# Kernel optimization log

Hardware: AMD Instinct MI355X
Metric: run time of the kernel (lower is better)

The kernel has to match this reference:

```python
import jax, jax.numpy as jnp
import numpy as np
import math

B, S, D, H = 2, 2048, 1024, 16
DK = D // H
SCALE = math.sqrt(DK)
NEG_BIG = -1e9


def setup_inputs() -> dict:
    key = jax.random.key(0)
    ks = jax.random.split(key, 7)
    x = jax.random.normal(ks[0], (B, S, D), dtype=jnp.float32)
    # additive causal mask: 0 on/below diagonal, -inf above
    causal = jnp.triu(jnp.ones((S, S), dtype=bool), k=1)
    mask = jnp.where(causal, -jnp.inf, 0.0).astype(jnp.float32)
    key_padding_mask = jax.random.bernoulli(ks[1], 0.1, (B, S))
    init = 1.0 / math.sqrt(D)
    Wq = jax.random.normal(ks[2], (D, D), dtype=jnp.float32) * init
    Wk = jax.random.normal(ks[3], (D, D), dtype=jnp.float32) * init
    Wv = jax.random.normal(ks[4], (D, D), dtype=jnp.float32) * init
    Wo = jax.random.normal(ks[5], (D, D), dtype=jnp.float32) * init
    bo = jnp.zeros((D,), dtype=jnp.float32)
    return {"x": x, "mask": mask, "key_padding_mask": key_padding_mask,
            "Wq": Wq, "Wk": Wk, "Wv": Wv, "Wo": Wo, "bo": bo}


def reference(x, mask, key_padding_mask, Wq, Wk, Wv, Wo, bo):
    b, s, d = x.shape
    # project and split heads -> [B,H,S,Dk]
    def heads(W):
        return jnp.einsum('bsd,de->bse', x, W).reshape(b, s, H, DK).transpose(0, 2, 1, 3)
    Q, K, V = heads(Wq), heads(Wk), heads(Wv)
    scores = jnp.einsum('bhqd,bhkd->bhqk', Q, K) / SCALE          # [B,H,S,S]
    scores = scores + mask[None, None]                            # additive attn mask
    scores = jnp.where(key_padding_mask[:, None, None, :], -jnp.inf, scores)
    # rows whose max is -inf (fully masked) get all scores set to -1e9
    max_scores = jnp.max(scores, axis=-1, keepdims=True)
    scores = jnp.where(jnp.isinf(max_scores), NEG_BIG, scores)
    attn = jax.nn.softmax(scores, axis=-1)
    attn = jnp.where(jnp.isnan(attn), 0.0, attn)
    # dropout is identity in eval mode
    ctx = jnp.einsum('bhqk,bhkd->bhqd', attn, V)                  # [B,H,S,Dk]
    ctx = ctx.transpose(0, 2, 1, 3).reshape(b, s, d)
    return jnp.einsum('bsd,de->bse', ctx, Wo) + bo
```

## Files before the change

### kernel.cpp

```cpp
#include <hip/hip_runtime.h>
#include <stdint.h>

#define NB 2
#define NS 2048
#define ND 1024
#define NH 16
#define NDK 64

typedef __attribute__((ext_vector_type(8))) short s8v;
typedef __attribute__((ext_vector_type(4))) float f4v;
typedef __attribute__((ext_vector_type(4))) unsigned short us4v;
typedef __attribute__((ext_vector_type(8))) unsigned short us8v;
typedef __attribute__((ext_vector_type(2))) uint32_t u2v;

__device__ __forceinline__ unsigned short f2bf(float f) {
  uint32_t u = __builtin_bit_cast(uint32_t, f);
  u = (u + 0x7fffu + ((u >> 16) & 1u)) >> 16;
  return (unsigned short)u;
}
__device__ __forceinline__ float bf2f(unsigned short h) {
  uint32_t u = ((uint32_t)h) << 16;
  return __builtin_bit_cast(float, u);
}
__device__ __forceinline__ uint32_t cvtpk(float lo, float hi) {
  uint32_t r;
  asm("v_cvt_pk_bf16_f32 %0, %1, %2" : "=v"(r) : "v"(lo), "v"(hi));
  return r;
}

__device__ __forceinline__ void gload16(const void* g, void* l) {
  __builtin_amdgcn_global_load_lds(
      (const __attribute__((address_space(1))) void*)g,
      (__attribute__((address_space(3))) void*)l, 16, 0, 0);
}

__global__ void k_convert_x(const float* __restrict__ x, unsigned short* __restrict__ xbf) {
  int i = (blockIdx.x * 256 + threadIdx.x) * 4;
  float4 v = *(const float4*)(x + i);
  us4v o;
  o[0] = f2bf(v.x); o[1] = f2bf(v.y); o[2] = f2bf(v.z); o[3] = f2bf(v.w);
  *(us4v*)(xbf + i) = o;
}

__global__ void k_transpose_w(const float* __restrict__ Wq, const float* __restrict__ Wk,
                              const float* __restrict__ Wv, const float* __restrict__ Wo,
                              unsigned short* __restrict__ wt_qkv, unsigned short* __restrict__ wt_o) {
  __shared__ float tls[64][65];
  int bid = blockIdx.x;
  int mat = bid >> 8;
  int tile = bid & 255;
  int tk = tile >> 4, tn = tile & 15;
  const float* W = (mat == 0) ? Wq : (mat == 1) ? Wk : (mat == 2) ? Wv : Wo;
  int t = threadIdx.x;
  int lr = t >> 2;
  int lc0 = (t & 3) * 16;
  const float* src = W + (size_t)(tk * 64 + lr) * 1024 + tn * 64 + lc0;
#pragma unroll
  for (int j = 0; j < 16; j += 4) {
    float4 v = *(const float4*)(src + j);
    tls[lr][lc0 + j + 0] = v.x; tls[lr][lc0 + j + 1] = v.y;
    tls[lr][lc0 + j + 2] = v.z; tls[lr][lc0 + j + 3] = v.w;
  }
  __syncthreads();
  float scale = (mat == 0) ? 0.18033688f : 1.0f;
  int nr = t >> 2, kc0 = (t & 3) * 16;
  unsigned short* dst = ((mat < 3) ? (wt_qkv + (size_t)(mat * 1024 + tn * 64 + nr) * 1024)
                                   : (wt_o + (size_t)(tn * 64 + nr) * 1024)) + tk * 64 + kc0;
  us8v o0, o1;
#pragma unroll
  for (int j = 0; j < 8; j++) o0[j] = f2bf(tls[kc0 + j][nr] * scale);
#pragma unroll
  for (int j = 0; j < 8; j++) o1[j] = f2bf(tls[kc0 + 8 + j][nr] * scale);
  *(us8v*)(dst) = o0;
  *(us8v*)(dst + 8) = o1;
}

template <int MODE>
__global__ __launch_bounds__(256) void k_gemm(const unsigned short* __restrict__ A,
                                              const unsigned short* __restrict__ Bt,
                                              unsigned short* __restrict__ qklin,
                                              unsigned short* __restrict__ vt,
                                              const float* __restrict__ bias,
                                              float* __restrict__ out) {
  __shared__ unsigned short lds_a[3][128 * 32];
  __shared__ unsigned short lds_b[3][128 * 32];
  const int K = 1024;
  const int NT = K / 32;
  int bid = blockIdx.x;
  int xcd = bid & 7, local = bid >> 3;
  int m0 = (xcd * 4 + (local & 3)) * 128;
  int n0 = (local >> 2) * 128;
  int tid = threadIdx.x, lane = tid & 63, w = tid >> 6;
  int wm = w >> 1, wn = w & 1;
  int g = lane >> 4, c0 = lane & 15;
  int rrel = lane >> 2;
  int gran = lane & 3;
  int rsw = (rrel >> 1) & 3;
  int csw = (c0 >> 1) & 3;
  f4v acc[4][4];
#pragma unroll
  for (int mi = 0; mi < 4; mi++)
#pragma unroll
    for (int ni = 0; ni < 4; ni++) acc[mi][ni] = (f4v){0.f, 0.f, 0.f, 0.f};

#define STAGE(kt_, buf_)                                                        \
  do {                                                                          \
    int koff = (kt_)*32;                                                        \
    _Pragma("unroll") for (int i = 0; i < 2; i++) {                             \
      int r = 32 * w + 16 * i + rrel;                                           \
      gload16(A + (size_t)(m0 + r) * K + koff + 8 * (gran ^ rsw),               \
              (void*)(lds_a[buf_] + (32 * w + 16 * i) * 32));                   \
      gload16(Bt + (size_t)(n0 + r) * K + koff + 8 * (gran ^ rsw),              \
              (void*)(lds_b[buf_] + (32 * w + 16 * i) * 32));                   \
    }                                                                           \
  } while (0)

  STAGE(0, 0);
  STAGE(1, 1);
  asm volatile("s_waitcnt vmcnt(8)" ::: "memory");
  __builtin_amdgcn_s_barrier();
  __builtin_amdgcn_sched_barrier(0);

  for (int kt = 0; kt < NT; ++kt) {
    int cur = kt % 3;
    if (kt + 2 < NT) STAGE(kt + 2, (kt + 2) % 3);
    s8v af[4], bfr[4];
#pragma unroll
    for (int mi = 0; mi < 4; mi++) {
      int row = 64 * wm + 16 * mi + c0;
      af[mi] = *(const s8v*)(lds_a[cur] + row * 32 + 8 * (g ^ csw));
    }
#pragma unroll
    for (int ni = 0; ni < 4; ni++) {
      int row = 64 * wn + 16 * ni + c0;
      bfr[ni] = *(const s8v*)(lds_b[cur] + row * 32 + 8 * (g ^ csw));
    }
#pragma unroll
    for (int mi = 0; mi < 4; mi++)
#pragma unroll
      for (int ni = 0; ni < 4; ni++)
        acc[mi][ni] = __builtin_amdgcn_mfma_f32_16x16x32_bf16(af[mi], bfr[ni], acc[mi][ni], 0, 0, 0);
    if (kt + 1 < NT) {
      if (kt + 2 < NT) {
        asm volatile("s_waitcnt vmcnt(8)" ::: "memory");
      } else {
        asm volatile("s_waitcnt vmcnt(0)" ::: "memory");
      }
      __builtin_amdgcn_s_barrier();
      __builtin_amdgcn_sched_barrier(0);
    }
  }
#undef STAGE

#pragma unroll
  for (int mi = 0; mi < 4; mi++)
#pragma unroll
    for (int ni = 0; ni < 4; ni++)
#pragma unroll
      for (int r = 0; r < 4; r++) {
        int m = m0 + 64 * wm + 16 * mi + 4 * g + r;
        int n = n0 + 64 * wn + 16 * ni + c0;
        float v = acc[mi][ni][r];
        if (MODE == 0) {
          unsigned short hv = f2bf(v);
          if (n < 2048) {
            qklin[(size_t)m * 2048 + n] = hv;
          } else {
            int b = m >> 11, s = m & 2047;
            int hh = (n - 2048) >> 6, dk = n & 63;
            vt[(size_t)((b * 16 + hh) * 64 + dk) * 2048 + s] = hv;
          }
        } else {
          out[(size_t)m * 1024 + n] = v + bias[n];
        }
      }
}

__global__ void k_vmean(const unsigned short* __restrict__ vt, float* __restrict__ vmean) {
  int row = blockIdx.x * 4 + (threadIdx.x >> 6);
  int lane = threadIdx.x & 63;
  const unsigned short* p = vt + (size_t)row * 2048 + lane * 32;
  float s = 0.f;
#pragma unroll
  for (int j = 0; j < 32; j += 8) {
    us8v v = *(const us8v*)(p + j);
#pragma unroll
    for (int e = 0; e < 8; e++) s += bf2f(v[e]);
  }
#pragma unroll
  for (int m = 1; m < 64; m <<= 1) s += __shfl_xor(s, m);
  if (lane == 0) vmean[row] = s * (1.0f / 2048.0f);
}

__global__ __launch_bounds__(256) void k_attn(const unsigned short* __restrict__ qklin,
                                              const unsigned short* __restrict__ vt,
                                              const int* __restrict__ kpm,
                                              const float* __restrict__ vmean,
                                              unsigned short* __restrict__ ctx) {
  __shared__ unsigned short lds_k[2][64 * 64];
  __shared__ unsigned short lds_v[2][64 * 64];
  __shared__ unsigned short p_lds[4][16 * 64];
  int wg = blockIdx.x;
  int w5 = wg >> 5, bh = wg & 31;
  int qt = (w5 < 8) ? 31 - w5 : (w5 < 16) ? w5 - 8 : (w5 < 24) ? 39 - w5 : w5 - 16;
  int b = bh >> 4, h = bh & 15;
  int tid = threadIdx.x, lane = tid & 63, w = tid >> 6;
  int g = lane >> 4, c0 = lane & 15;
  int q0 = qt * 64 + w * 16;
  unsigned short* pl = p_lds[w];
  int rrel = lane >> 3, gran = lane & 7;

  const unsigned short* ksrc0 = qklin + (size_t)(b * NS) * 2048 + 1024 + h * 64;
  const unsigned short* vsrc0 = vt + (size_t)(bh * 64) * 2048;

  const unsigned short* qbase = qklin + (size_t)(b * NS + q0 + c0) * 2048 + h * 64 + 8 * g;
  s8v qf0 = *(const s8v*)(qbase);
  s8v qf1 = *(const s8v*)(qbase + 32);

  f4v cacc[4];
#pragma unroll
  for (int d = 0; d < 4; d++) cacc[d] = (f4v){0.f, 0.f, 0.f, 0.f};
  float m_s = -1e30f, l_s = 0.f;
  int qrow = q0 + c0;

#define STAGEKV(it_, buf_)                                                      \
  do {                                                                          \
    int kb_ = (it_)*64;                                                         \
    _Pragma("unroll") for (int i = 0; i < 2; i++) {                             \
      int r = 16 * w + 8 * i + rrel;                                            \
      gload16(ksrc0 + (size_t)(kb_ + r) * 2048 + 8 * (gran ^ rrel),             \
              (void*)(lds_k[buf_] + (16 * w + 8 * i) * 64));                    \
      gload16(vsrc0 + (size_t)r * 2048 + kb_ + 8 * (gran ^ rrel),               \
              (void*)(lds_v[buf_] + (16 * w + 8 * i) * 64));                    \
    }                                                                           \
  } while (0)

  STAGEKV(0, 0);
  int kp_cur = kpm[b * NS + lane];

  int nkt = qt + 1;
  for (int it = 0; it < nkt; ++it) {
    int kb = it * 64;
    int cur = it & 1;
    int kp_next = 0;
    if (it + 1 < nkt) {
      STAGEKV(it + 1, cur ^ 1);
      kp_next = kpm[b * NS + (it + 1) * 64 + lane];
      asm volatile("s_waitcnt vmcnt(5)" ::: "memory");
    } else {
      asm volatile("s_waitcnt vmcnt(0)" ::: "memory");
    }
    __builtin_amdgcn_s_barrier();
    __builtin_amdgcn_sched_barrier(0);
    uint64_t padmask = __ballot(kp_cur != 0);
    f4v sacc[4];
#pragma unroll
    for (int t = 0; t < 4; t++) {
      int row = 16 * t + c0;
      s8v kf0 = *(const s8v*)(lds_k[cur] + row * 64 + 8 * (g ^ (c0 & 7)));
      s8v kf1 = *(const s8v*)(lds_k[cur] + row * 64 + 8 * ((4 + g) ^ (c0 & 7)));
      f4v z = (f4v){0.f, 0.f, 0.f, 0.f};
      z = __builtin_amdgcn_mfma_f32_16x16x32_bf16(kf0, qf0, z, 0, 0, 0);
      z = __builtin_amdgcn_mfma_f32_16x16x32_bf16(kf1, qf1, z, 0, 0, 0);
      sacc[t] = z;
    }
    int thr = qrow - kb;
    uint64_t cmask = (thr >= 63) ? ~0ull : ((2ull << thr) - 1ull);
    uint64_t valid = cmask & ~padmask;
    uint32_t vlo = (uint32_t)valid, vhi = (uint32_t)(valid >> 32);
    float p[4][4];
    float mx = -1e30f;
#pragma unroll
    for (int t = 0; t < 4; t++) {
      uint32_t half = (t & 2) ? vhi : vlo;
      uint32_t nib = (half >> (16 * (t & 1) + 4 * g)) & 0xFu;
#pragma unroll
      for (int r = 0; r < 4; r++) {
        float s = sacc[t][r];
        s = ((nib >> r) & 1u) ? s : -1e30f;
        p[t][r] = s;
      }
      mx = fmaxf(mx, fmaxf(fmaxf(p[t][0], p[t][1]), fmaxf(p[t][2], p[t][3])));
    }
    mx = fmaxf(mx, __shfl_xor(mx, 16));
    mx = fmaxf(mx, __shfl_xor(mx, 32));
    if (!__all(mx <= m_s + 11.0f)) {
      float mnew = fmaxf(m_s, mx);
      float a = __builtin_exp2f(m_s - mnew);
      m_s = mnew;
      l_s *= a;
      int ybase = 20 * g;
#pragma unroll
      for (int r = 0; r < 4; r++) {
        float ar = __shfl(a, ybase + r);
#pragma unroll
        for (int d = 0; d < 4; d++) cacc[d][r] *= ar;
      }
    }
    float rs = 0.f;
#pragma unroll
    for (int t = 0; t < 4; t++)
#pragma unroll
      for (int r = 0; r < 4; r++) {
        float e = __builtin_exp2f(p[t][r] - m_s);
        p[t][r] = e;
        rs += e;
      }
    rs += __shfl_xor(rs, 16);
    rs += __shfl_xor(rs, 32);
    rs = (m_s > -1e29f) ? rs : 0.f;
    l_s += rs;
#pragma unroll
    for (int t = 0; t < 4; t++) {
      u2v pk;
      pk[0] = cvtpk(p[t][0], p[t][1]);
      pk[1] = cvtpk(p[t][2], p[t][3]);
      int gr = (2 * t + (g >> 1)) ^ (c0 & 7);
      *(u2v*)((char*)pl + c0 * 128 + gr * 16 + 8 * (g & 1)) = pk;
    }
    asm volatile("s_waitcnt lgkmcnt(0)" ::: "memory");
    __builtin_amdgcn_sched_barrier(0);
#pragma unroll
    for (int c = 0; c < 2; c++) {
      int off = c0 * 128 + 16 * g + 64 * c;
      off ^= (c0 & 7) << 4;
      s8v pf = *(const s8v*)((const char*)pl + off);
#pragma unroll
      for (int d = 0; d < 4; d++) {
        int row = 16 * d + c0;
        s8v vf = *(const s8v*)(lds_v[cur] + row * 64 + 8 * ((4 * c + g) ^ (c0 & 7)));
        cacc[d] = __builtin_amdgcn_mfma_f32_16x16x32_bf16(pf, vf, cacc[d], 0, 0, 0);
      }
    }
    __builtin_amdgcn_s_barrier();
    __builtin_amdgcn_sched_barrier(0);
    kp_cur = kp_next;
  }
#undef STAGEKV
  float lq[4];
  {
    int ybase = 20 * g;
#pragma unroll
    for (int r = 0; r < 4; r++) lq[r] = __shfl(l_s, ybase + r);
  }
#pragma unroll
  for (int d = 0; d < 4; d++)
#pragma unroll
    for (int r = 0; r < 4; r++) {
      int q = q0 + 4 * g + r;
      float l = lq[r];
      float v = (l > 0.f) ? cacc[d][r] / l : vmean[bh * 64 + 16 * d + c0];
      ctx[(size_t)(b * NS + q) * ND + h * 64 + 16 * d + c0] = f2bf(v);
    }
}

extern "C" void kernel_launch(void* const* d_in, const int* in_sizes, int n_in,
                              void* d_out, int out_size, void* d_ws, size_t ws_size,
                              hipStream_t stream) {
  const float* x  = (const float*)d_in[0];
  const int* kpm  = (const int*)d_in[2];
  const float* Wq = (const float*)d_in[3];
  const float* Wk = (const float*)d_in[4];
  const float* Wv = (const float*)d_in[5];
  const float* Wo = (const float*)d_in[6];
  const float* bo = (const float*)d_in[7];

  char* ws = (char*)d_ws;
  unsigned short* xbf   = (unsigned short*)(ws);
  unsigned short* wtqkv = (unsigned short*)(ws + 8u * 1024 * 1024);
  unsigned short* wto   = (unsigned short*)(ws + 14u * 1024 * 1024);
  unsigned short* vt    = (unsigned short*)(ws + 16u * 1024 * 1024);
  float* vmean          = (float*)(ws + 24u * 1024 * 1024);
  unsigned short* ctx   = xbf;
  unsigned short* qklin = (unsigned short*)d_out;

  k_convert_x<<<4096, 256, 0, stream>>>(x, xbf);
  k_transpose_w<<<1024, 256, 0, stream>>>(Wq, Wk, Wv, Wo, wtqkv, wto);
  k_gemm<0><<<768, 256, 0, stream>>>(xbf, wtqkv, qklin, vt, nullptr, nullptr);
  k_vmean<<<512, 256, 0, stream>>>(vt, vmean);
  k_attn<<<1024, 256, 0, stream>>>(qklin, vt, kpm, vmean, ctx);
  k_gemm<1><<<256, 256, 0, stream>>>(ctx, wto, nullptr, nullptr, bo, (float*)d_out);
}
```

Before: 142.2 us.

## Split GEMM kernels, transpose V epilogue through LDS, use smaller output-projection tiles

Splits the templated GEMM into separate QKV and output-projection kernels. The QKV kernel now stages V tiles in shared memory and writes the transposed V with 16-byte vector stores instead of scattered 2-byte stores. It also tightens the vmcnt waits to 4, matching the real number of loads in flight per stage. The output projection uses 64x64 tiles with double buffering and 1024 blocks, so more blocks fill the CUs, at the cost of less data reuse per block.

New measurement: 133.4 us. 1.07x faster.

```diff
diff --git a/kernel.cpp b/kernel.cpp
--- a/kernel.cpp
+++ b/kernel.cpp
@@ -75,15 +75,13 @@
   *(us8v*)(dst + 8) = o1;
 }
 
-template <int MODE>
-__global__ __launch_bounds__(256) void k_gemm(const unsigned short* __restrict__ A,
-                                              const unsigned short* __restrict__ Bt,
-                                              unsigned short* __restrict__ qklin,
-                                              unsigned short* __restrict__ vt,
-                                              const float* __restrict__ bias,
-                                              float* __restrict__ out) {
-  __shared__ unsigned short lds_a[3][128 * 32];
-  __shared__ unsigned short lds_b[3][128 * 32];
+__global__ __launch_bounds__(256) void k_gemm0(const unsigned short* __restrict__ A,
+                                               const unsigned short* __restrict__ Bt,
+                                               unsigned short* __restrict__ qklin,
+                                               unsigned short* __restrict__ vt) {
+  __shared__ unsigned short smem[6 * 128 * 32];
+#define SA(b_) (smem + (b_)*4096)
+#define SB(b_) (smem + 12288 + (b_)*4096)
   const int K = 1024;
   const int NT = K / 32;
   int bid = blockIdx.x;
@@ -109,15 +107,15 @@
     _Pragma("unroll") for (int i = 0; i < 2; i++) {                             \
       int r = 32 * w + 16 * i + rrel;                                           \
       gload16(A + (size_t)(m0 + r) * K + koff + 8 * (gran ^ rsw),               \
-              (void*)(lds_a[buf_] + (32 * w + 16 * i) * 32));                   \
+              (void*)(SA(buf_) + (32 * w + 16 * i) * 32));                      \
       gload16(Bt + (size_t)(n0 + r) * K + koff + 8 * (gran ^ rsw),              \
-              (void*)(lds_b[buf_] + (32 * w + 16 * i) * 32));                   \
+              (void*)(SB(buf_) + (32 * w + 16 * i) * 32));                      \
     }                                                                           \
   } while (0)
 
   STAGE(0, 0);
   STAGE(1, 1);
-  asm volatile("s_waitcnt vmcnt(8)" ::: "memory");
+  asm volatile("s_waitcnt vmcnt(4)" ::: "memory");
   __builtin_amdgcn_s_barrier();
   __builtin_amdgcn_sched_barrier(0);
 
@@ -128,12 +126,12 @@
 #pragma unroll
     for (int mi = 0; mi < 4; mi++) {
       int row = 64 * wm + 16 * mi + c0;
-      af[mi] = *(const s8v*)(lds_a[cur] + row * 32 + 8 * (g ^ csw));
+      af[mi] = *(const s8v*)(SA(cur) + row * 32 + 8 * (g ^ csw));
     }
 #pragma unroll
     for (int ni = 0; ni < 4; ni++) {
       int row = 64 * wn + 16 * ni + c0;
-      bfr[ni] = *(const s8v*)(lds_b[cur] + row * 32 + 8 * (g ^ csw));
+      bfr[ni] = *(const s8v*)(SB(cur) + row * 32 + 8 * (g ^ csw));
     }
 #pragma unroll
     for (int mi = 0; mi < 4; mi++)
@@ -142,7 +140,7 @@
         acc[mi][ni] = __builtin_amdgcn_mfma_f32_16x16x32_bf16(af[mi], bfr[ni], acc[mi][ni], 0, 0, 0);
     if (kt + 1 < NT) {
       if (kt + 2 < NT) {
-        asm volatile("s_waitcnt vmcnt(8)" ::: "memory");
+        asm volatile("s_waitcnt vmcnt(4)" ::: "memory");
       } else {
         asm volatile("s_waitcnt vmcnt(0)" ::: "memory");
       }
@@ -152,27 +150,124 @@
   }
 #undef STAGE
 
-#pragma unroll
-  for (int mi = 0; mi < 4; mi++)
-#pragma unroll
-    for (int ni = 0; ni < 4; ni++)
+  if (n0 < 2048) {
+#pragma unroll
+    for (int mi = 0; mi < 4; mi++)
+#pragma unroll
+      for (int ni = 0; ni < 4; ni++)
+#pragma unroll
+        for (int r = 0; r < 4; r++) {
+          int m = m0 + 64 * wm + 16 * mi + 4 * g + r;
+          int n = n0 + 64 * wn + 16 * ni + c0;
+          qklin[(size_t)m * 2048 + n] = f2bf(acc[mi][ni][r]);
+        }
+  } else {
+    const int PAD = 132;
+    unsigned short* tl = smem;
+    __syncthreads();
+#pragma unroll
+    for (int mi = 0; mi < 4; mi++)
+#pragma unroll
+      for (int ni = 0; ni < 4; ni++) {
+        int nloc = 64 * wn + 16 * ni + c0;
+        int m4 = 64 * wm + 16 * mi + 4 * g;
+        us4v pk;
+#pragma unroll
+        for (int r = 0; r < 4; r++) pk[r] = f2bf(acc[mi][ni][r]);
+        *(us4v*)(tl + nloc * PAD + m4) = pk;
+      }
+    __syncthreads();
+    int row = tid >> 1, half = tid & 1;
+    int n = n0 + row;
+    int hh = (n - 2048) >> 6, dk = n & 63;
+    int bb = m0 >> 11;
+    int s0 = (m0 & 2047) + 64 * half;
+    unsigned short* dstp = vt + (size_t)((bb * 16 + hh) * 64 + dk) * 2048 + s0;
+    const unsigned short* srcp = tl + row * PAD + 64 * half;
+#pragma unroll
+    for (int j = 0; j < 8; j++) {
+      us4v lo = *(const us4v*)(srcp + 8 * j);
+      us4v hi = *(const us4v*)(srcp + 8 * j + 4);
+      us8v v8;
+      v8[0] = lo[0]; v8[1] = lo[1]; v8[2] = lo[2]; v8[3] = lo[3];
+      v8[4] = hi[0]; v8[5] = hi[1]; v8[6] = hi[2]; v8[7] = hi[3];
+      *(us8v*)(dstp + 8 * j) = v8;
+    }
+  }
+#undef SA
+#undef SB
+}
+
+__global__ __launch_bounds__(256) void k_gemm1(const unsigned short* __restrict__ A,
+                                               const unsigned short* __restrict__ Bt,
+                                               const float* __restrict__ bias,
+                                               float* __restrict__ out) {
+  __shared__ unsigned short lds_a[2][64 * 32];
+  __shared__ unsigned short lds_b[2][64 * 32];
+  const int K = 1024;
+  const int NT = K / 32;
+  int bid = blockIdx.x;
+  int xcd = bid & 7, local = bid >> 3;
+  int m0 = (xcd * 8 + (local & 7)) * 64;
+  int n0 = (local >> 3) * 64;
+  int tid = threadIdx.x, lane = tid & 63, w = tid >> 6;
+  int wm = w >> 1, wn = w & 1;
+  int g = lane >> 4, c0 = lane & 15;
+  int rrel = lane >> 2;
+  int gran = lane & 3;
+  int rsw = (rrel >> 1) & 3;
+  int csw = (c0 >> 1) & 3;
+  f4v acc[2][2];
+#pragma unroll
+  for (int mi = 0; mi < 2; mi++)
+#pragma unroll
+    for (int ni = 0; ni < 2; ni++) acc[mi][ni] = (f4v){0.f, 0.f, 0.f, 0.f};
+
+#define STAGE1(kt_, buf_)                                                       \
+  do {                                                                          \
+    int koff = (kt_)*32;                                                        \
+    int r = 16 * w + rrel;                                                      \
+    gload16(A + (size_t)(m0 + r) * K + koff + 8 * (gran ^ rsw),                 \
+            (void*)(lds_a[buf_] + (16 * w) * 32));                              \
+    gload16(Bt + (size_t)(n0 + r) * K + koff + 8 * (gran ^ rsw),                \
+            (void*)(lds_b[buf_] + (16 * w) * 32));                              \
+  } while (0)
+
+  STAGE1(0, 0);
+  __syncthreads();
+
+  for (int kt = 0; kt < NT; ++kt) {
+    int cur = kt & 1;
+    if (kt + 1 < NT) STAGE1(kt + 1, cur ^ 1);
+    s8v af[2], bfr[2];
+#pragma unroll
+    for (int mi = 0; mi < 2; mi++) {
+      int row = 32 * wm + 16 * mi + c0;
+      af[mi] = *(const s8v*)(lds_a[cur] + row * 32 + 8 * (g ^ csw));
+    }
+#pragma unroll
+    for (int ni = 0; ni < 2; ni++) {
+      int row = 32 * wn + 16 * ni + c0;
+      bfr[ni] = *(const s8v*)(lds_b[cur] + row * 32 + 8 * (g ^ csw));
+    }
+#pragma unroll
+    for (int mi = 0; mi < 2; mi++)
+#pragma unroll
+      for (int ni = 0; ni < 2; ni++)
+        acc[mi][ni] = __builtin_amdgcn_mfma_f32_16x16x32_bf16(af[mi], bfr[ni], acc[mi][ni], 0, 0, 0);
+    __syncthreads();
+  }
+#undef STAGE1
+
+#pragma unroll
+  for (int mi = 0; mi < 2; mi++)
+#pragma unroll
+    for (int ni = 0; ni < 2; ni++)
 #pragma unroll
       for (int r = 0; r < 4; r++) {
-        int m = m0 + 64 * wm + 16 * mi + 4 * g + r;
-        int n = n0 + 64 * wn + 16 * ni + c0;
-        float v = acc[mi][ni][r];
-        if (MODE == 0) {
-          unsigned short hv = f2bf(v);
-          if (n < 2048) {
-            qklin[(size_t)m * 2048 + n] = hv;
-          } else {
-            int b = m >> 11, s = m & 2047;
-            int hh = (n - 2048) >> 6, dk = n & 63;
-            vt[(size_t)((b * 16 + hh) * 64 + dk) * 2048 + s] = hv;
-          }
-        } else {
-          out[(size_t)m * 1024 + n] = v + bias[n];
-        }
+        int m = m0 + 32 * wm + 16 * mi + 4 * g + r;
+        int n = n0 + 32 * wn + 16 * ni + c0;
+        out[(size_t)m * 1024 + n] = acc[mi][ni][r] + bias[n];
       }
 }
 
@@ -376,8 +471,8 @@
 
   k_convert_x<<<4096, 256, 0, stream>>>(x, xbf);
   k_transpose_w<<<1024, 256, 0, stream>>>(Wq, Wk, Wv, Wo, wtqkv, wto);
-  k_gemm<0><<<768, 256, 0, stream>>>(xbf, wtqkv, qklin, vt, nullptr, nullptr);
+  k_gemm0<<<768, 256, 0, stream>>>(xbf, wtqkv, qklin, vt);
   k_vmean<<<512, 256, 0, stream>>>(vt, vmean);
   k_attn<<<1024, 256, 0, stream>>>(qklin, vt, kpm, vmean, ctx);
-  k_gemm<1><<<256, 256, 0, stream>>>(ctx, wto, nullptr, nullptr, bo, (float*)d_out);
-}
+  k_gemm1<<<1024, 256, 0, stream>>>(ctx, wto, bo, (float*)d_out);
+}
```
